# Performance work log

Hardware: AMD Instinct MI355X
Metric: run time of the kernel (lower is better)

## Reference

```python
import jax, jax.numpy as jnp
import numpy as np

SENTENCE_NUMBER = 32
UNITS = 50
WORD_DIM = 100   # 2 * MIDDLE_OUTPUT
USER_DIM = 100   # 2 * USER_VEC_DIM
B, T = 256, 2048


def setup_inputs() -> dict:
    key = jax.random.key(0)
    ks = jax.random.split(key, 6)
    return {
        "sentence_batch": jax.random.normal(ks[0], (B, T, WORD_DIM), dtype=jnp.float32),
        "user_vec_batch": jax.random.normal(ks[1], (B, USER_DIM), dtype=jnp.float32),
        "vw": jax.random.normal(ks[2], (UNITS, 1), dtype=jnp.float32) * 0.05,
        "wh": jax.random.normal(ks[3], (UNITS, WORD_DIM), dtype=jnp.float32) * 0.05,
        "wu": jax.random.normal(ks[4], (UNITS, USER_DIM), dtype=jnp.float32) * 0.05,
        "bw": jax.random.normal(ks[5], (UNITS, 1), dtype=jnp.float32) * 0.05,
    }


def reference(sentence_batch, user_vec_batch, vw, wh, wu, bw):
    # Additive attention per word, softmax within each sentence section,
    # weighted-sum pooling of words -> one vector per sentence.
    b, t, d = sentence_batch.shape
    s = SENTENCE_NUMBER
    sec = t // s
    # batched projections (replaces per-word (units x 1) matmuls)
    wh_proj = jnp.einsum("btd,ud->btu", sentence_batch, wh)          # [B,T,units]
    wu_proj = jnp.einsum("bd,ud->bu", user_vec_batch, wu) + bw[:, 0]  # [B,units]
    tan = jnp.tanh(wh_proj + wu_proj[:, None, :])                    # [B,T,units]
    e = tan @ vw[:, 0]                                               # [B,T]
    # softmax over words within each sentence section
    e = e.reshape(b, s, sec)
    alpha = jax.nn.softmax(e, axis=-1)                               # [B,S,sec]
    words = sentence_batch.reshape(b, s, sec, d)
    # weighted-sum pooling -> document of sentence vectors
    return jnp.einsum("bsw,bswd->bsd", alpha, words)                 # [B,S,D]
```

## Files before the change

### kernel.cpp

```cpp
#include <hip/hip_runtime.h>
#include <hip/hip_bf16.h>

#define B_   256
#define T_   2048
#define D_   100
#define U_   50
#define S_   32
#define SEC_ 64

typedef __attribute__((ext_vector_type(8))) short short8;
typedef __attribute__((ext_vector_type(4))) float f32x4;

__device__ __forceinline__ float fast_tanh(float x) {
    float e = __expf(2.0f * x);
    return 1.0f - 2.0f * __builtin_amdgcn_rcpf(1.0f + e);
}

__device__ __forceinline__ short f2bf(float f) {
    union { __hip_bfloat16 h; unsigned short u; } cv;
    cv.h = __float2bfloat16(f);
    return (short)cv.u;
}

__device__ __forceinline__ short8 pack8(f32x4 a, f32x4 b) {
    short8 r;
    r[0] = f2bf(a[0]); r[1] = f2bf(a[1]); r[2] = f2bf(a[2]); r[3] = f2bf(a[3]);
    r[4] = f2bf(b[0]); r[5] = f2bf(b[1]); r[6] = f2bf(b[2]); r[7] = f2bf(b[3]);
    return r;
}

__global__ __launch_bounds__(64) void wu_proj_kernel(
    const float* __restrict__ user_vec, const float* __restrict__ wu,
    const float* __restrict__ bw, float* __restrict__ wup) {
    int b = blockIdx.x;
    int u = threadIdx.x;
    if (u >= U_) return;
    const f32x4* uv4 = reinterpret_cast<const f32x4*>(user_vec + b * D_);
    const f32x4* wu4 = reinterpret_cast<const f32x4*>(wu + u * D_);
    float acc = 0.f;
#pragma unroll
    for (int c = 0; c < D_ / 4; ++c) {
        f32x4 a = uv4[c];
        f32x4 w = wu4[c];
        acc = __builtin_fmaf(a[0], w[0], acc);
        acc = __builtin_fmaf(a[1], w[1], acc);
        acc = __builtin_fmaf(a[2], w[2], acc);
        acc = __builtin_fmaf(a[3], w[3], acc);
    }
    wup[b * U_ + u] = acc + bw[u];
}

#define LOADX(X, mm) do {                                                \
    const float* row_ = secbase + (16 * (mm) + li) * D_;                 \
    X[0] = *reinterpret_cast<const f32x4*>(row_ + c0);                   \
    X[1] = *reinterpret_cast<const f32x4*>(row_ + c0 + 16);              \
    X[2] = *reinterpret_cast<const f32x4*>(row_ + c0 + 32);              \
    X[3] = *reinterpret_cast<const f32x4*>(row_ + c0 + 48);              \
    X[4] = *reinterpret_cast<const f32x4*>(row_ + c0 + 64);              \
    X[5] = *reinterpret_cast<const f32x4*>(row_ + c0 + 80);              \
    X[6] = *reinterpret_cast<const f32x4*>(row_ + 96) * mg;              \
} while (0)

#define COMPUTE_M(X) do {                                                \
    short8 af[4];                                                        \
    af[0] = pack8(X[0], X[1]);                                           \
    af[1] = pack8(X[2], X[3]);                                           \
    af[2] = pack8(X[4], X[5]);                                           \
    af[3] = pack8(X[6], zero4);                                          \
    f32x4 acc[4];                                                        \
    _Pragma("unroll")                                                    \
    for (int n = 0; n < 4; ++n) acc[n] = (f32x4){0.f, 0.f, 0.f, 0.f};    \
    _Pragma("unroll")                                                    \
    for (int ks = 0; ks < 4; ++ks) {                                     \
        _Pragma("unroll")                                                \
        for (int n = 0; n < 4; ++n) {                                    \
            acc[n] = __builtin_amdgcn_mfma_f32_16x16x32_bf16(            \
                af[ks], whb[n * 4 + ks][l], acc[n], 0, 0, 0);            \
        }                                                                \
    }                                                                    \
    float p[4];                                                          \
    _Pragma("unroll")                                                    \
    for (int r = 0; r < 4; ++r) {                                        \
        float t = 0.f;                                                   \
        _Pragma("unroll")                                                \
        for (int n = 0; n < 4; ++n)                                      \
            t = __builtin_fmaf(vwl[n], fast_tanh(acc[n][r] + gl[n]), t); \
        t += __shfl_xor(t, 1);                                           \
        t += __shfl_xor(t, 2);                                           \
        t += __shfl_xor(t, 4);                                           \
        t += __shfl_xor(t, 8);                                           \
        p[r] = __expf(t - Mb);                                           \
    }                                                                    \
    tsum += (p[0] + p[1]) + (p[2] + p[3]);                               \
    const int src = (li >> 2) << 4;                                      \
    const float w0 = __shfl(p[0], src);                                  \
    const float w1 = __shfl(p[1], src);                                  \
    const float w2 = __shfl(p[2], src);                                  \
    const float w3 = __shfl(p[3], src);                                  \
    const float wa = (li & 1) ? w1 : w0;                                 \
    const float wb = (li & 1) ? w3 : w2;                                 \
    const float wgt = (li & 2) ? wb : wa;                                \
    _Pragma("unroll")                                                    \
    for (int j = 0; j < 7; ++j)                                          \
        pool[j] = pool[j] + X[j] * wgt;                                  \
} while (0)

__global__ __launch_bounds__(256, 4) void attn_pool_v7(
    const float* __restrict__ sent,
    const float* __restrict__ vw,
    const float* __restrict__ wh,
    const float* __restrict__ wup_all,
    float* __restrict__ out) {
    __shared__ short8 whb[16][64];
    __shared__ float  pbuf[2][2][128];
    __shared__ float  tsb[2][2];

    const int tid = threadIdx.x;
    const int wid = tid >> 6;
    const int l   = tid & 63;
    const int g   = l >> 4;
    const int li  = l & 15;
    const int p   = wid >> 1;
    const int h   = wid & 1;

    const int b = blockIdx.x >> 4;
    const int s = (blockIdx.x & 15) * 2 + p;
    const float* secbase = sent + ((size_t)b * T_ + (size_t)s * SEC_) * D_;
    const float* wup = wup_all + b * U_;

    const float mg = (g == 0) ? 1.f : 0.f;
    const int c0 = 4 * g;
    const f32x4 zero4 = (f32x4){0.f, 0.f, 0.f, 0.f};

    f32x4 xA[7], xB[7];
    LOADX(xA, 2 * h);
    LOADX(xB, 2 * h + 1);

#pragma unroll
    for (int j = 0; j < 4; ++j) {
        const int idx = tid + 256 * j;
        const int pli = idx & 15;
        const int pg  = (idx >> 4) & 3;
        const int pks = (idx >> 6) & 3;
        const int pn  = idx >> 8;
        const int u   = 16 * pn + pli;
        const bool uv = (u < U_);
        const int k0  = 32 * pks + 4 * pg;
        const bool v1 = uv && (k0 <= D_ - 4);
        const bool v2 = uv && (k0 + 16 <= D_ - 4);
        const float* rowp = wh + (uv ? u : 0) * D_;
        f32x4 a = *reinterpret_cast<const f32x4*>(rowp + (v1 ? k0 : 0));
        f32x4 bb = *reinterpret_cast<const f32x4*>(rowp + (v2 ? k0 + 16 : 0));
        a  *= (v1 ? 1.f : 0.f);
        bb *= (v2 ? 1.f : 0.f);
        whb[idx >> 6][idx & 63] = pack8(a, bb);
    }

    float vwl[4], gl[4];
#pragma unroll
    for (int n = 0; n < 4; ++n) {
        const int uu = 16 * n + li;
        const bool uv = (uu < U_);
        const int uc = uv ? uu : 0;
        const float rv = uv ? 1.f : 0.f;
        vwl[n] = vw[uc] * rv;
        gl[n]  = wup[uc] * rv;
    }
    float Mb = fabsf(vwl[0]) + fabsf(vwl[1]) + fabsf(vwl[2]) + fabsf(vwl[3]);
    Mb += __shfl_xor(Mb, 1);
    Mb += __shfl_xor(Mb, 2);
    Mb += __shfl_xor(Mb, 4);
    Mb += __shfl_xor(Mb, 8);
    __syncthreads();

    f32x4 pool[7];
#pragma unroll
    for (int j = 0; j < 7; ++j) pool[j] = zero4;
    float tsum = 0.f;

    COMPUTE_M(xA);
    COMPUTE_M(xB);

    tsum += __shfl_xor(tsum, 16);
    tsum += __shfl_xor(tsum, 32);

#pragma unroll
    for (int j = 0; j < 7; ++j) {
#pragma unroll
        for (int c = 0; c < 4; ++c) {
            float v = pool[j][c];
            v += __shfl_xor(v, 1);
            v += __shfl_xor(v, 2);
            v += __shfl_xor(v, 4);
            v += __shfl_xor(v, 8);
            pool[j][c] = v;
        }
    }

    if (li == 0) {
#pragma unroll
        for (int j = 0; j < 6; ++j) {
#pragma unroll
            for (int c = 0; c < 4; ++c) {
                const int k = 32 * (j >> 1) + 16 * (j & 1) + 4 * g + c;
                pbuf[p][h][k] = pool[j][c];
            }
        }
        if (g == 0) {
#pragma unroll
            for (int c = 0; c < 4; ++c) pbuf[p][h][96 + c] = pool[6][c];
        }
    }
    if (l == 0) tsb[p][h] = tsum;
    __syncthreads();

    if (h == 0) {
        const float inv = 1.0f / (tsb[p][0] + tsb[p][1]);
        float* po = out + ((size_t)b * S_ + s) * D_;
        po[l] = (pbuf[p][0][l] + pbuf[p][1][l]) * inv;
        if (l < D_ - SEC_)
            po[SEC_ + l] = (pbuf[p][0][SEC_ + l] + pbuf[p][1][SEC_ + l]) * inv;
    }
}

extern "C" void kernel_launch(void* const* d_in, const int* in_sizes, int n_in,
                              void* d_out, int out_size, void* d_ws, size_t ws_size,
                              hipStream_t stream) {
    const float* sent = (const float*)d_in[0];
    const float* uvec = (const float*)d_in[1];
    const float* vw   = (const float*)d_in[2];
    const float* wh   = (const float*)d_in[3];
    const float* wu   = (const float*)d_in[4];
    const float* bw   = (const float*)d_in[5];
    float* out = (float*)d_out;
    float* wup = (float*)d_ws;

    wu_proj_kernel<<<dim3(B_), dim3(64), 0, stream>>>(uvec, wu, bw, wup);
    attn_pool_v7<<<dim3(B_ * S_ / 2), dim3(256), 0, stream>>>(sent, vw, wh, wup, out);
}
```

Measured before the change: 52.07 us.

## Give each wave two whole sections with register double-buffered loads

```diff
diff --git a/kernel.cpp b/kernel.cpp
--- a/kernel.cpp
+++ b/kernel.cpp
@@ -50,8 +50,8 @@
     wup[b * U_ + u] = acc + bw[u];
 }
 
-#define LOADX(X, mm) do {                                                \
-    const float* row_ = secbase + (16 * (mm) + li) * D_;                 \
+#define LOADX(X, base, mm) do {                                          \
+    const float* row_ = (base) + (16 * (mm) + li) * D_;                  \
     X[0] = *reinterpret_cast<const f32x4*>(row_ + c0);                   \
     X[1] = *reinterpret_cast<const f32x4*>(row_ + c0 + 16);              \
     X[2] = *reinterpret_cast<const f32x4*>(row_ + c0 + 32);              \
@@ -105,36 +105,77 @@
         pool[j] = pool[j] + X[j] * wgt;                                  \
 } while (0)
 
-__global__ __launch_bounds__(256, 4) void attn_pool_v7(
+#define EPILOG(PO) do {                                                  \
+    float ts = tsum;                                                     \
+    ts += __shfl_xor(ts, 16);                                            \
+    ts += __shfl_xor(ts, 32);                                            \
+    _Pragma("unroll")                                                    \
+    for (int j = 0; j < 7; ++j) {                                        \
+        _Pragma("unroll")                                                \
+        for (int c = 0; c < 4; ++c) {                                    \
+            float v = pool[j][c];                                        \
+            v += __shfl_xor(v, 1);                                       \
+            v += __shfl_xor(v, 2);                                       \
+            v += __shfl_xor(v, 4);                                       \
+            v += __shfl_xor(v, 8);                                       \
+            pool[j][c] = v;                                              \
+        }                                                                \
+    }                                                                    \
+    const float inv_ = 1.0f / ts;                                        \
+    if (li == 0) {                                                       \
+        _Pragma("unroll")                                                \
+        for (int j = 0; j < 6; ++j) {                                    \
+            _Pragma("unroll")                                            \
+            for (int c = 0; c < 4; ++c) {                                \
+                const int k = 32 * (j >> 1) + 16 * (j & 1) + 4 * g + c;  \
+                poolbuf[wid][k] = pool[j][c];                            \
+            }                                                            \
+        }                                                                \
+        if (g == 0) {                                                    \
+            _Pragma("unroll")                                            \
+            for (int c = 0; c < 4; ++c) poolbuf[wid][96 + c] = pool[6][c]; \
+        }                                                                \
+    }                                                                    \
+    asm volatile("s_waitcnt lgkmcnt(0)" ::: "memory");                   \
+    {                                                                    \
+        float* po_ = (PO);                                               \
+        po_[l] = poolbuf[wid][l] * inv_;                                 \
+        if (l < D_ - SEC_) po_[SEC_ + l] = poolbuf[wid][SEC_ + l] * inv_; \
+    }                                                                    \
+    _Pragma("unroll")                                                    \
+    for (int j = 0; j < 7; ++j) pool[j] = zero4;                         \
+    tsum = 0.f;                                                          \
+} while (0)
+
+__global__ __launch_bounds__(256, 2) void attn_pool_v8(
     const float* __restrict__ sent,
     const float* __restrict__ vw,
     const float* __restrict__ wh,
     const float* __restrict__ wup_all,
     float* __restrict__ out) {
     __shared__ short8 whb[16][64];
-    __shared__ float  pbuf[2][2][128];
-    __shared__ float  tsb[2][2];
+    __shared__ float  poolbuf[4][128];
 
     const int tid = threadIdx.x;
     const int wid = tid >> 6;
     const int l   = tid & 63;
     const int g   = l >> 4;
     const int li  = l & 15;
-    const int p   = wid >> 1;
-    const int h   = wid & 1;
-
-    const int b = blockIdx.x >> 4;
-    const int s = (blockIdx.x & 15) * 2 + p;
-    const float* secbase = sent + ((size_t)b * T_ + (size_t)s * SEC_) * D_;
-    const float* wup = wup_all + b * U_;
+
+    const int W  = blockIdx.x * 4 + wid;
+    const int b  = W >> 4;
+    const int sp = W & 15;
+    const float* sec0 = sent + ((size_t)b * T_ + (size_t)(2 * sp) * SEC_) * D_;
+    const float* sec1 = sec0 + SEC_ * D_;
+    const float* wup  = wup_all + b * U_;
 
     const float mg = (g == 0) ? 1.f : 0.f;
     const int c0 = 4 * g;
     const f32x4 zero4 = (f32x4){0.f, 0.f, 0.f, 0.f};
 
     f32x4 xA[7], xB[7];
-    LOADX(xA, 2 * h);
-    LOADX(xB, 2 * h + 1);
+    LOADX(xA, sec0, 0);
+    LOADX(xB, sec0, 1);
 
 #pragma unroll
     for (int j = 0; j < 4; ++j) {
@@ -149,7 +190,7 @@
         const bool v1 = uv && (k0 <= D_ - 4);
         const bool v2 = uv && (k0 + 16 <= D_ - 4);
         const float* rowp = wh + (uv ? u : 0) * D_;
-        f32x4 a = *reinterpret_cast<const f32x4*>(rowp + (v1 ? k0 : 0));
+        f32x4 a  = *reinterpret_cast<const f32x4*>(rowp + (v1 ? k0 : 0));
         f32x4 bb = *reinterpret_cast<const f32x4*>(rowp + (v2 ? k0 + 16 : 0));
         a  *= (v1 ? 1.f : 0.f);
         bb *= (v2 ? 1.f : 0.f);
@@ -178,49 +219,19 @@
     for (int j = 0; j < 7; ++j) pool[j] = zero4;
     float tsum = 0.f;
 
+    float* po0 = out + ((size_t)b * S_ + 2 * sp) * D_;
+    float* po1 = po0 + D_;
+
+    COMPUTE_M(xA); LOADX(xA, sec0, 2);
+    COMPUTE_M(xB); LOADX(xB, sec0, 3);
+    COMPUTE_M(xA); LOADX(xA, sec1, 0);
+    COMPUTE_M(xB); LOADX(xB, sec1, 1);
+    EPILOG(po0);
+    COMPUTE_M(xA); LOADX(xA, sec1, 2);
+    COMPUTE_M(xB); LOADX(xB, sec1, 3);
     COMPUTE_M(xA);
     COMPUTE_M(xB);
-
-    tsum += __shfl_xor(tsum, 16);
-    tsum += __shfl_xor(tsum, 32);
-
-#pragma unroll
-    for (int j = 0; j < 7; ++j) {
-#pragma unroll
-        for (int c = 0; c < 4; ++c) {
-            float v = pool[j][c];
-            v += __shfl_xor(v, 1);
-            v += __shfl_xor(v, 2);
-            v += __shfl_xor(v, 4);
-            v += __shfl_xor(v, 8);
-            pool[j][c] = v;
-        }
-    }
-
-    if (li == 0) {
-#pragma unroll
-        for (int j = 0; j < 6; ++j) {
-#pragma unroll
-            for (int c = 0; c < 4; ++c) {
-                const int k = 32 * (j >> 1) + 16 * (j & 1) + 4 * g + c;
-                pbuf[p][h][k] = pool[j][c];
-            }
-        }
-        if (g == 0) {
-#pragma unroll
-            for (int c = 0; c < 4; ++c) pbuf[p][h][96 + c] = pool[6][c];
-        }
-    }
-    if (l == 0) tsb[p][h] = tsum;
-    __syncthreads();
-
-    if (h == 0) {
-        const float inv = 1.0f / (tsb[p][0] + tsb[p][1]);
-        float* po = out + ((size_t)b * S_ + s) * D_;
-        po[l] = (pbuf[p][0][l] + pbuf[p][1][l]) * inv;
-        if (l < D_ - SEC_)
-            po[SEC_ + l] = (pbuf[p][0][SEC_ + l] + pbuf[p][1][SEC_ + l]) * inv;
-    }
+    EPILOG(po1);
 }
 
 extern "C" void kernel_launch(void* const* d_in, const int* in_sizes, int n_in,
@@ -236,5 +247,5 @@
     float* wup = (float*)d_ws;
 
     wu_proj_kernel<<<dim3(B_), dim3(64), 0, stream>>>(uvec, wu, bw, wup);
-    attn_pool_v7<<<dim3(B_ * S_ / 2), dim3(256), 0, stream>>>(sent, vw, wh, wup, out);
-}
+    attn_pool_v8<<<dim3(B_ * S_ / 8), dim3(256), 0, stream>>>(sent, vw, wh, wup, out);
+}
```

Result: slower. 53.93 us (+3.6%).
